# Kernel tuning notes

Hardware: AMD Instinct MI355X
Metric: run time of the kernel (lower is better)

## Reference

```python
import jax, jax.numpy as jnp
import numpy as np

B, L, D = 128, 512, 512   # batch, len_max, encoder feature dim
E, H, V = 64, 512, 17     # label emb size, hidden size, label vocab
PAD = 0                   # entl_pad_value


def setup_inputs() -> dict:
    key = jax.random.key(0)
    ks = jax.random.split(key, 6)
    inputs = jax.random.normal(ks[0], (B, L, D), dtype=jnp.float32)
    emb_table = jax.random.normal(ks[1], (V, E), dtype=jnp.float32) * 0.02
    # xavier_uniform with tanh gain for ht1
    gain = 5.0 / 3.0
    limit1 = gain * np.sqrt(6.0 / (D + E + H))
    W1 = jax.random.uniform(ks[2], (H, D + E), dtype=jnp.float32,
                            minval=-limit1, maxval=limit1)
    b1 = jnp.zeros((H,), dtype=jnp.float32)
    limit2 = np.sqrt(1.0 / H)
    W2 = jax.random.uniform(ks[3], (V, H), dtype=jnp.float32,
                            minval=-limit2, maxval=limit2)
    b2 = jax.random.uniform(ks[4], (V,), dtype=jnp.float32,
                            minval=-limit2, maxval=limit2)
    return {"inputs": inputs, "emb_table": emb_table,
            "W1": W1, "b1": b1, "W2": W2, "b2": b2}


def reference(inputs, emb_table, W1, b1, W2, b2):
    # padding_idx row is identically zero (as in nn.Embedding(padding_idx=PAD))
    table = emb_table.at[PAD].set(0.0)

    def step(prev_emb, x_t):
        # x_t: [B, D], prev_emb: [B, E]
        x = jnp.concatenate([x_t, prev_emb], axis=-1)          # [B, D+E]
        h = jnp.tanh(x @ W1.T + b1)                            # [B, H]
        logit = h @ W2.T + b2                                  # [B, V]
        logp = jax.nn.log_softmax(logit, axis=-1)              # [B, V]
        pred = jnp.argmax(logp, axis=-1)                       # [B] int
        emb = table[pred]                                      # [B, E]
        return emb, (logit, pred, logp, emb)

    init_emb = jnp.broadcast_to(table[PAD], (inputs.shape[0], E))
    xs = jnp.swapaxes(inputs, 0, 1)                            # [L, B, D]
    _, (logits, preds, probs, preds_emb) = jax.lax.scan(step, init_emb, xs)
    # stack along time -> move time to dim 1
    logits = jnp.swapaxes(logits, 0, 1)       # [B, L, V]
    preds = jnp.swapaxes(preds, 0, 1)         # [B, L]
    probs = jnp.swapaxes(probs, 0, 1)         # [B, L, V]
    preds_emb = jnp.swapaxes(preds_emb, 0, 1) # [B, L, E]
    return logits, preds, probs, preds_emb
```

## Files before the change

kernel.cpp:

```cpp
#include <hip/hip_runtime.h>
#include <math.h>

#define B_ 128
#define L_ 512
#define D_ 512
#define E_ 64
#define H_ 512
#define V_ 17

#define LOG2E_F 1.4426950408889634f
#define LN2_F   0.6931471805599453f

__device__ __forceinline__ float fast_tanh(float x) {
  float e = __builtin_amdgcn_exp2f(x * (2.0f * LOG2E_F));
  return 1.0f - 2.0f * __builtin_amdgcn_rcpf(e + 1.0f);
}

__global__ void dh_kernel(const float* __restrict__ W1, const float* __restrict__ table,
                          float* __restrict__ TD) {
  int h = threadIdx.x;
  float w[E_];
#pragma unroll
  for (int e = 0; e < E_; ++e) w[e] = W1[h * (D_ + E_) + D_ + e];
  TD[h] = 0.f;
  for (int v = 1; v < V_; ++v) {
    float acc = 0.f;
#pragma unroll
    for (int e = 0; e < E_; ++e) acc += w[e] * table[v * E_ + e];
    TD[v * H_ + h] = fast_tanh(acc);
  }
}

#define GBM 128
#define GBN 128
#define GBK 32
#define PITCH 20
#define SCALE_A 1024.0f
#define SCALE_W 256.0f
#define INV_SCALE (1.0f / (1024.0f * 256.0f))

typedef _Float16 half8 __attribute__((ext_vector_type(8)));
typedef __fp16 fp16x2 __attribute__((ext_vector_type(2)));
typedef float float4v __attribute__((ext_vector_type(4)));

union H8u { half8 h; fp16x2 p[4]; };

__device__ __forceinline__ uint4 split4(float4 v, float scale) {
  float a0 = v.x * scale, a1 = v.y * scale, a2 = v.z * scale, a3 = v.w * scale;
  _Float16 h0 = (_Float16)a0, h1 = (_Float16)a1, h2 = (_Float16)a2, h3 = (_Float16)a3;
  _Float16 l0 = (_Float16)(a0 - (float)h0), l1 = (_Float16)(a1 - (float)h1);
  _Float16 l2 = (_Float16)(a2 - (float)h2), l3 = (_Float16)(a3 - (float)h3);
  union { _Float16 h; unsigned short u; } c;
  unsigned int hu0, hu1, hu2, hu3, lu0, lu1, lu2, lu3;
  c.h = h0; hu0 = c.u; c.h = h1; hu1 = c.u; c.h = h2; hu2 = c.u; c.h = h3; hu3 = c.u;
  c.h = l0; lu0 = c.u; c.h = l1; lu1 = c.u; c.h = l2; lu2 = c.u; c.h = l3; lu3 = c.u;
  uint4 r;
  r.x = hu0 | (hu1 << 16);
  r.y = hu2 | (hu3 << 16);
  r.z = lu0 | (lu1 << 16);
  r.w = lu2 | (lu3 << 16);
  return r;
}

__global__ __launch_bounds__(256)
void wsplit_kernel(const float* __restrict__ W1, unsigned int* __restrict__ WHI,
                   unsigned int* __restrict__ WLO) {
  const int idx = blockIdx.x * 256 + threadIdx.x;
  const int row = idx >> 7, c4 = idx & 127;
  const float4 wv = *(const float4*)&W1[(size_t)row * (D_ + E_) + 4 * c4];
  const uint4 pw = split4(wv, SCALE_W);
  *(uint2*)&WHI[row * 256 + 2 * c4] = make_uint2(pw.x, pw.y);
  *(uint2*)&WLO[row * 256 + 2 * c4] = make_uint2(pw.z, pw.w);
}

__global__ __launch_bounds__(256, 2)
void gemm_kernel(const float* __restrict__ A, const unsigned int* __restrict__ WHI,
                 const unsigned int* __restrict__ WLO,
                 const float* __restrict__ b1, float* __restrict__ TZ) {
  __shared__ unsigned int Ahi[GBM * PITCH], Alo[GBM * PITCH];
  __shared__ unsigned int Whi[GBN * PITCH], Wlo[GBN * PITCH];

  const int t = threadIdx.x;
  const int ln = t & 63, w = t >> 6;
  const int wm = w & 1, wn = w >> 1;
  const int mBase = blockIdx.x * GBM;
  const int nBase = blockIdx.y * GBN;
  const int lrow = ln & 15, lquad = ln >> 4;

  float4v acc[4][4];
#pragma unroll
  for (int i = 0; i < 4; ++i)
#pragma unroll
    for (int j = 0; j < 4; ++j) acc[i][j] = (float4v){0.f, 0.f, 0.f, 0.f};

  for (int kt = 0; kt < D_; kt += GBK) {
#pragma unroll
    for (int q = 0; q < 4; ++q) {
      const int idx = q * 256 + t;
      const int m = idx >> 3, f = idx & 7;
      const float4 av = *(const float4*)&A[(size_t)(mBase + m) * D_ + kt + 4 * f];
      const uint4 pa = split4(av, SCALE_A);
      *(uint2*)&Ahi[m * PITCH + 2 * f] = make_uint2(pa.x, pa.y);
      *(uint2*)&Alo[m * PITCH + 2 * f] = make_uint2(pa.z, pa.w);
      const uint2 wh = *(const uint2*)&WHI[(nBase + m) * 256 + (kt >> 1) + 2 * f];
      const uint2 wl = *(const uint2*)&WLO[(nBase + m) * 256 + (kt >> 1) + 2 * f];
      *(uint2*)&Whi[m * PITCH + 2 * f] = wh;
      *(uint2*)&Wlo[m * PITCH + 2 * f] = wl;
    }
    __syncthreads();

    half8 ah[4], al[4], bh[4], bl[4];
#pragma unroll
    for (int tm = 0; tm < 4; ++tm) {
      const int off = (wm * 64 + tm * 16 + lrow) * PITCH + 4 * lquad;
      ah[tm] = *(const half8*)&Ahi[off];
      al[tm] = *(const half8*)&Alo[off];
    }
#pragma unroll
    for (int tn = 0; tn < 4; ++tn) {
      const int off = (wn * 64 + tn * 16 + lrow) * PITCH + 4 * lquad;
      bh[tn] = *(const half8*)&Whi[off];
      bl[tn] = *(const half8*)&Wlo[off];
    }
#pragma unroll
    for (int tm = 0; tm < 4; ++tm)
#pragma unroll
      for (int tn = 0; tn < 4; ++tn) {
        acc[tm][tn] = __builtin_amdgcn_mfma_f32_16x16x32_f16(ah[tm], bh[tn], acc[tm][tn], 0, 0, 0);
        acc[tm][tn] = __builtin_amdgcn_mfma_f32_16x16x32_f16(ah[tm], bl[tn], acc[tm][tn], 0, 0, 0);
        acc[tm][tn] = __builtin_amdgcn_mfma_f32_16x16x32_f16(al[tm], bh[tn], acc[tm][tn], 0, 0, 0);
      }
    __syncthreads();
  }

#pragma unroll
  for (int tn = 0; tn < 4; ++tn) {
    const int col = nBase + wn * 64 + tn * 16 + lrow;
    const float bv = b1[col];
#pragma unroll
    for (int tm = 0; tm < 4; ++tm) {
      const int row0 = mBase + wm * 64 + tm * 16 + lquad * 4;
#pragma unroll
      for (int r = 0; r < 4; ++r)
        TZ[(size_t)(row0 + r) * H_ + col] = fast_tanh(acc[tm][tn][r] * INV_SCALE + bv);
    }
  }
}

#define LG_ROWS 32
#define ZP 516
#define WP 260

__global__ __launch_bounds__(512, 2)
void lg_kernel(const float* Zin, const float* __restrict__ TD,
               const float* __restrict__ W2, const float* __restrict__ b2,
               float* G) {
  __shared__ float sTZ[LG_ROWS * ZP];
  __shared__ float sTD[V_ * ZP];
  __shared__ unsigned int sW2hi[16 * WP];
  __shared__ unsigned int sW2lo[16 * WP];
  __shared__ float sW16[H_];
  __shared__ float sS[8][16][20];
  __shared__ unsigned char nb[LG_ROWS][32];

  const int t = threadIdx.x;
  const int ln = t & 63, w = t >> 6;
  const int bt0 = blockIdx.x * LG_ROWS;

#pragma unroll
  for (int i = 0; i < 8; ++i) {
    const int f = t + 512 * i;
    const int r = f >> 7, c = (f & 127) * 4;
    *(float4*)&sTZ[r * ZP + c] = *(const float4*)&Zin[(size_t)(bt0 + r) * H_ + c];
  }
#pragma unroll
  for (int i = 0; i < 5; ++i) {
    const int f = t + 512 * i;
    if (f < (V_ * H_ / 4)) {
      const int r = f >> 7, c = (f & 127) * 4;
      *(float4*)&sTD[r * ZP + c] = *(const float4*)&TD[(size_t)r * H_ + c];
    }
  }
#pragma unroll
  for (int i = 0; i < 4; ++i) {
    const int f = t + 512 * i;
    const int r = f >> 7, c4 = f & 127;
    const float4 wv = *(const float4*)&W2[(size_t)r * H_ + 4 * c4];
    const uint4 pw = split4(wv, SCALE_W);
    *(uint2*)&sW2hi[r * WP + 2 * c4] = make_uint2(pw.x, pw.y);
    *(uint2*)&sW2lo[r * WP + 2 * c4] = make_uint2(pw.z, pw.w);
  }
  if (t < 128) *(float4*)&sW16[t * 4] = *(const float4*)&W2[(size_t)16 * H_ + t * 4];
  __syncthreads();

  const int lrow = ln & 15, lq = ln >> 4;
  const float b2a = b2[lrow];
  const float b2c = b2[16];

  for (int task = w; task < 34; task += 8) {
    const int rg = (task >= 17) ? 1 : 0;
    const int p = task - rg * 17;
    const int rbase = rg * 16;

    float4v acc0 = (float4v){0.f, 0.f, 0.f, 0.f};
    float p16 = 0.f;
    for (int kt = 0; kt < H_; kt += 32) {
      const float* zr = &sTZ[(rbase + lrow) * ZP + kt + lq * 8];
      const float* dr = &sTD[p * ZP + kt + lq * 8];
      float a[8];
#pragma unroll
      for (int j = 0; j < 8; ++j) {
        const float tz = zr[j], td = dr[j];
        const float r = __builtin_amdgcn_rcpf(fmaf(tz, td, 1.0f) * 0.0009765625f);
        a[j] = (tz + td) * r;
      }
      H8u uh, ul;
#pragma unroll
      for (int jj = 0; jj < 4; ++jj) {
        const fp16x2 hp = __builtin_amdgcn_cvt_pkrtz(a[2 * jj], a[2 * jj + 1]);
        uh.p[jj] = hp;
        ul.p[jj] = __builtin_amdgcn_cvt_pkrtz(a[2 * jj] - (float)hp.x,
                                              a[2 * jj + 1] - (float)hp.y);
      }
      const int wo = (kt >> 1) + lq * 4;
      const half8 bh0 = *(const half8*)&sW2hi[lrow * WP + wo];
      const half8 bl0 = *(const half8*)&sW2lo[lrow * WP + wo];
      acc0 = __builtin_amdgcn_mfma_f32_16x16x32_f16(uh.h, bh0, acc0, 0, 0, 0);
      acc0 = __builtin_amdgcn_mfma_f32_16x16x32_f16(uh.h, bl0, acc0, 0, 0, 0);
      acc0 = __builtin_amdgcn_mfma_f32_16x16x32_f16(ul.h, bh0, acc0, 0, 0, 0);
      const float* wr = &sW16[kt + lq * 8];
#pragma unroll
      for (int j = 0; j < 8; ++j) p16 = fmaf(a[j], wr[j], p16);
    }
    p16 += __shfl_xor(p16, 16, 64);
    p16 += __shfl_xor(p16, 32, 64);
#pragma unroll
    for (int r = 0; r < 4; ++r)
      sS[w][lq * 4 + r][lrow] = acc0[r] * INV_SCALE + b2a;
    if (ln < 16) {
      float va[17];
      const float4 q0 = *(const float4*)&sS[w][ln][0];
      const float4 q1 = *(const float4*)&sS[w][ln][4];
      const float4 q2 = *(const float4*)&sS[w][ln][8];
      const float4 q3 = *(const float4*)&sS[w][ln][12];
      va[0] = q0.x; va[1] = q0.y; va[2] = q0.z; va[3] = q0.w;
      va[4] = q1.x; va[5] = q1.y; va[6] = q1.z; va[7] = q1.w;
      va[8] = q2.x; va[9] = q2.y; va[10] = q2.z; va[11] = q2.w;
      va[12] = q3.x; va[13] = q3.y; va[14] = q3.z; va[15] = q3.w;
      va[16] = p16 * (1.0f / 1024.0f) + b2c;
      float m = va[0]; int am = 0;
#pragma unroll
      for (int i = 1; i < 17; ++i) if (va[i] > m) { m = va[i]; am = i; }
      float* gs = &G[(size_t)(bt0 + rbase + ln) * H_ + p * 20];
      *(float4*)&gs[0] = q0; *(float4*)&gs[4] = q1;
      *(float4*)&gs[8] = q2; *(float4*)&gs[12] = q3;
      gs[16] = va[16];
      nb[rbase + ln][p] = (unsigned char)am;
    }
  }
  __syncthreads();
  if (t < 160) {
    const int row = t / 5, d = t % 5;
    ((unsigned int*)&G[(size_t)(bt0 + row) * H_ + 352])[d] =
        *(const unsigned int*)&nb[row][d * 4];
  }
}

__global__ __launch_bounds__(64, 1)
void chase_kernel(const float* __restrict__ G, float* __restrict__ out_preds) {
  __shared__ unsigned char nxt[L_ * 32];
  const int b = blockIdx.x, ln = threadIdx.x;
#pragma unroll
  for (int i = 0; i < 8; ++i) {
    const int tt = ln + 64 * i;
    const unsigned int* src = (const unsigned int*)&G[((size_t)b * L_ + tt) * H_ + 352];
    *(uint4*)&nxt[tt * 32] = *(const uint4*)src;
    *(unsigned int*)&nxt[tt * 32 + 16] = src[4];
  }
  __syncthreads();
  int pred = 0;
  float* op = out_preds + (size_t)b * L_;
  for (int tt = 0; tt < L_; ++tt) {
    pred = nxt[tt * 32 + pred];
    if (ln == 0) op[tt] = (float)pred;
  }
}

__global__ __launch_bounds__(256)
void epi_kernel(const float* __restrict__ G, const float* __restrict__ table,
                const float* __restrict__ preds,
                float* __restrict__ out_logits, float* __restrict__ out_probs,
                float* __restrict__ out_pemb) {
  const int bt = blockIdx.x * 256 + threadIdx.x;
  const int tt = bt & (L_ - 1);
  const int p = (tt == 0) ? 0 : (int)preds[bt - 1];
  const float* g = &G[(size_t)bt * H_ + p * 20];
  float va[17];
  {
    const float4 q0 = *(const float4*)&g[0];
    const float4 q1 = *(const float4*)&g[4];
    const float4 q2 = *(const float4*)&g[8];
    const float4 q3 = *(const float4*)&g[12];
    va[0] = q0.x; va[1] = q0.y; va[2] = q0.z; va[3] = q0.w;
    va[4] = q1.x; va[5] = q1.y; va[6] = q1.z; va[7] = q1.w;
    va[8] = q2.x; va[9] = q2.y; va[10] = q2.z; va[11] = q2.w;
    va[12] = q3.x; va[13] = q3.y; va[14] = q3.z; va[15] = q3.w;
    va[16] = g[16];
  }
  float m = va[0];
#pragma unroll
  for (int i = 1; i < 17; ++i) m = fmaxf(m, va[i]);
  float s = 0.f;
#pragma unroll
  for (int i = 0; i < 17; ++i) s += __builtin_amdgcn_exp2f((va[i] - m) * LOG2E_F);
  const float lse = __builtin_amdgcn_logf(s) * LN2_F;
  float* lo = out_logits + (size_t)bt * V_;
  float* pb = out_probs + (size_t)bt * V_;
#pragma unroll
  for (int i = 0; i < 17; ++i) { lo[i] = va[i]; pb[i] = va[i] - m - lse; }
  const int pr = (int)preds[bt];
  float* pe = out_pemb + (size_t)bt * E_;
  if (pr == 0) {
#pragma unroll
    for (int i = 0; i < 16; ++i) *(float4*)&pe[4 * i] = (float4){0.f, 0.f, 0.f, 0.f};
  } else {
    const float* tr = &table[(size_t)pr * E_];
#pragma unroll
    for (int i = 0; i < 16; ++i) *(float4*)&pe[4 * i] = *(const float4*)&tr[4 * i];
  }
}

extern "C" void kernel_launch(void* const* d_in, const int* in_sizes, int n_in,
                              void* d_out, int out_size, void* d_ws, size_t ws_size,
                              hipStream_t stream) {
  const float* inputs = (const float*)d_in[0];
  const float* table  = (const float*)d_in[1];
  const float* W1     = (const float*)d_in[2];
  const float* b1     = (const float*)d_in[3];
  const float* W2     = (const float*)d_in[4];
  const float* b2     = (const float*)d_in[5];

  float* out = (float*)d_out;
  float* out_logits = out;
  float* out_preds  = out_logits + (size_t)B_ * L_ * V_;
  float* out_probs  = out_preds + (size_t)B_ * L_;
  float* out_pemb   = out_probs + (size_t)B_ * L_ * V_;

  float* TD = (float*)d_ws;
  float* TZ = (float*)((char*)d_ws + 65536);

  unsigned int* WHI = (unsigned int*)out_pemb;
  unsigned int* WLO = WHI + 512 * 256;

  dh_kernel<<<1, 512, 0, stream>>>(W1, table, TD);
  wsplit_kernel<<<256, 256, 0, stream>>>(W1, WHI, WLO);
  dim3 g(65536 / GBM, H_ / GBN);
  gemm_kernel<<<g, 256, 0, stream>>>(inputs, WHI, WLO, b1, TZ);
  lg_kernel<<<65536 / LG_ROWS, 512, 0, stream>>>(TZ, TD, W2, b2, TZ);
  chase_kernel<<<B_, 64, 0, stream>>>(TZ, out_preds);
  epi_kernel<<<65536 / 256, 256, 0, stream>>>(TZ, table, out_preds,
                                              out_logits, out_probs, out_pemb);
}
```

Baseline: 572.8 us.

## Widen GEMM tile to full N and rework logit kernel with fp16 tanh-addition expansion

The hidden GEMM now uses 512-thread blocks that each compute all 512 output columns for 128 rows, so every A tile is loaded and split once per block instead of once per N-block. The logit kernel stores the tanh activations pre-split into fp16 hi/lo parts plus a derivative term. It replaces the per-element fp32 reciprocal of the tanh-addition formula with an fp16 series correction added to the low part, and precomputes the base row-16 dot product once per row. Each wave now processes up to five label candidates with a shared A fragment. This cuts VALU work and reloads, at the cost of more registers and LDS and of reduced accuracy from the fp16 polynomial approximation.

```diff
diff --git a/kernel.cpp b/kernel.cpp
--- a/kernel.cpp
+++ b/kernel.cpp
@@ -31,9 +31,6 @@
   }
 }
 
-#define GBM 128
-#define GBN 128
-#define GBK 32
 #define PITCH 20
 #define SCALE_A 1024.0f
 #define SCALE_W 256.0f
@@ -43,7 +40,7 @@
 typedef __fp16 fp16x2 __attribute__((ext_vector_type(2)));
 typedef float float4v __attribute__((ext_vector_type(4)));
 
-union H8u { half8 h; fp16x2 p[4]; };
+union H8c { half8 h; fp16x2 q[4]; unsigned int u[4]; uint4 u4; };
 
 __device__ __forceinline__ uint4 split4(float4 v, float scale) {
   float a0 = v.x * scale, a1 = v.y * scale, a2 = v.z * scale, a3 = v.w * scale;
@@ -62,6 +59,14 @@
   return r;
 }
 
+__device__ __forceinline__ uint2 pack4h(_Float16 a, _Float16 b, _Float16 c, _Float16 d) {
+  union { _Float16 h; unsigned short u; } x;
+  unsigned int lo, hi;
+  x.h = a; lo = x.u; x.h = b; lo |= ((unsigned int)x.u) << 16;
+  x.h = c; hi = x.u; x.h = d; hi |= ((unsigned int)x.u) << 16;
+  return make_uint2(lo, hi);
+}
+
 __global__ __launch_bounds__(256)
 void wsplit_kernel(const float* __restrict__ W1, unsigned int* __restrict__ WHI,
                    unsigned int* __restrict__ WLO) {
@@ -73,43 +78,45 @@
   *(uint2*)&WLO[row * 256 + 2 * c4] = make_uint2(pw.z, pw.w);
 }
 
-__global__ __launch_bounds__(256, 2)
+__global__ __launch_bounds__(512, 2)
 void gemm_kernel(const float* __restrict__ A, const unsigned int* __restrict__ WHI,
                  const unsigned int* __restrict__ WLO,
                  const float* __restrict__ b1, float* __restrict__ TZ) {
-  __shared__ unsigned int Ahi[GBM * PITCH], Alo[GBM * PITCH];
-  __shared__ unsigned int Whi[GBN * PITCH], Wlo[GBN * PITCH];
+  __shared__ unsigned int Ahi[128 * PITCH], Alo[128 * PITCH];
+  __shared__ unsigned int Whi[512 * PITCH], Wlo[512 * PITCH];
 
   const int t = threadIdx.x;
   const int ln = t & 63, w = t >> 6;
   const int wm = w & 1, wn = w >> 1;
-  const int mBase = blockIdx.x * GBM;
-  const int nBase = blockIdx.y * GBN;
+  const int mBase = blockIdx.x * 128;
   const int lrow = ln & 15, lquad = ln >> 4;
 
-  float4v acc[4][4];
+  float4v acc[4][8];
 #pragma unroll
   for (int i = 0; i < 4; ++i)
 #pragma unroll
-    for (int j = 0; j < 4; ++j) acc[i][j] = (float4v){0.f, 0.f, 0.f, 0.f};
-
-  for (int kt = 0; kt < D_; kt += GBK) {
-#pragma unroll
-    for (int q = 0; q < 4; ++q) {
-      const int idx = q * 256 + t;
+    for (int j = 0; j < 8; ++j) acc[i][j] = (float4v){0.f, 0.f, 0.f, 0.f};
+
+  for (int kt = 0; kt < D_; kt += 32) {
+#pragma unroll
+    for (int q = 0; q < 2; ++q) {
+      const int idx = q * 512 + t;
       const int m = idx >> 3, f = idx & 7;
       const float4 av = *(const float4*)&A[(size_t)(mBase + m) * D_ + kt + 4 * f];
       const uint4 pa = split4(av, SCALE_A);
       *(uint2*)&Ahi[m * PITCH + 2 * f] = make_uint2(pa.x, pa.y);
       *(uint2*)&Alo[m * PITCH + 2 * f] = make_uint2(pa.z, pa.w);
-      const uint2 wh = *(const uint2*)&WHI[(nBase + m) * 256 + (kt >> 1) + 2 * f];
-      const uint2 wl = *(const uint2*)&WLO[(nBase + m) * 256 + (kt >> 1) + 2 * f];
-      *(uint2*)&Whi[m * PITCH + 2 * f] = wh;
-      *(uint2*)&Wlo[m * PITCH + 2 * f] = wl;
+    }
+#pragma unroll
+    for (int q = 0; q < 4; ++q) {
+      const int idx = q * 512 + t;
+      const int n = idx >> 2, d4 = (idx & 3) * 4;
+      *(uint4*)&Whi[n * PITCH + d4] = *(const uint4*)&WHI[n * 256 + (kt >> 1) + d4];
+      *(uint4*)&Wlo[n * PITCH + d4] = *(const uint4*)&WLO[n * 256 + (kt >> 1) + d4];
     }
     __syncthreads();
 
-    half8 ah[4], al[4], bh[4], bl[4];
+    half8 ah[4], al[4];
 #pragma unroll
     for (int tm = 0; tm < 4; ++tm) {
       const int off = (wm * 64 + tm * 16 + lrow) * PITCH + 4 * lquad;
@@ -117,25 +124,23 @@
       al[tm] = *(const half8*)&Alo[off];
     }
 #pragma unroll
-    for (int tn = 0; tn < 4; ++tn) {
-      const int off = (wn * 64 + tn * 16 + lrow) * PITCH + 4 * lquad;
-      bh[tn] = *(const half8*)&Whi[off];
-      bl[tn] = *(const half8*)&Wlo[off];
-    }
-#pragma unroll
-    for (int tm = 0; tm < 4; ++tm)
-#pragma unroll
-      for (int tn = 0; tn < 4; ++tn) {
-        acc[tm][tn] = __builtin_amdgcn_mfma_f32_16x16x32_f16(ah[tm], bh[tn], acc[tm][tn], 0, 0, 0);
-        acc[tm][tn] = __builtin_amdgcn_mfma_f32_16x16x32_f16(ah[tm], bl[tn], acc[tm][tn], 0, 0, 0);
-        acc[tm][tn] = __builtin_amdgcn_mfma_f32_16x16x32_f16(al[tm], bh[tn], acc[tm][tn], 0, 0, 0);
+    for (int tn = 0; tn < 8; ++tn) {
+      const int off = (wn * 128 + tn * 16 + lrow) * PITCH + 4 * lquad;
+      const half8 bh = *(const half8*)&Whi[off];
+      const half8 bl = *(const half8*)&Wlo[off];
+#pragma unroll
+      for (int tm = 0; tm < 4; ++tm) {
+        acc[tm][tn] = __builtin_amdgcn_mfma_f32_16x16x32_f16(ah[tm], bh, acc[tm][tn], 0, 0, 0);
+        acc[tm][tn] = __builtin_amdgcn_mfma_f32_16x16x32_f16(ah[tm], bl, acc[tm][tn], 0, 0, 0);
+        acc[tm][tn] = __builtin_amdgcn_mfma_f32_16x16x32_f16(al[tm], bh, acc[tm][tn], 0, 0, 0);
       }
+    }
     __syncthreads();
   }
 
 #pragma unroll
-  for (int tn = 0; tn < 4; ++tn) {
-    const int col = nBase + wn * 64 + tn * 16 + lrow;
+  for (int tn = 0; tn < 8; ++tn) {
+    const int col = wn * 128 + tn * 16 + lrow;
     const float bv = b1[col];
 #pragma unroll
     for (int tm = 0; tm < 4; ++tm) {
@@ -147,38 +152,54 @@
   }
 }
 
-#define LG_ROWS 32
-#define ZP 516
+#define LGR 32
+#define AP 520
 #define WP 260
 
 __global__ __launch_bounds__(512, 2)
 void lg_kernel(const float* Zin, const float* __restrict__ TD,
                const float* __restrict__ W2, const float* __restrict__ b2,
                float* G) {
-  __shared__ float sTZ[LG_ROWS * ZP];
-  __shared__ float sTD[V_ * ZP];
-  __shared__ unsigned int sW2hi[16 * WP];
-  __shared__ unsigned int sW2lo[16 * WP];
-  __shared__ float sW16[H_];
-  __shared__ float sS[8][16][20];
-  __shared__ unsigned char nb[LG_ROWS][32];
+  __shared__ __align__(16) unsigned int sAhiD[LGR * AP / 2];
+  __shared__ __align__(16) unsigned int sAloD[LGR * AP / 2];
+  __shared__ __align__(16) unsigned int sUD[LGR * AP / 2];
+  __shared__ __align__(16) unsigned int sTDd[V_ * 256];
+  __shared__ __align__(16) unsigned int sW2hi[16 * WP];
+  __shared__ __align__(16) unsigned int sW2lo[16 * WP];
+  __shared__ __align__(16) unsigned int sW16hi[256];
+  __shared__ __align__(16) unsigned int sW16lo[256];
+  __shared__ __align__(16) float sS[8][16][20];
+  __shared__ __align__(16) float sV16b[32];
+  __shared__ __align__(16) unsigned char nb[LGR][20];
 
   const int t = threadIdx.x;
   const int ln = t & 63, w = t >> 6;
-  const int bt0 = blockIdx.x * LG_ROWS;
+  const int bt0 = blockIdx.x * LGR;
 
 #pragma unroll
   for (int i = 0; i < 8; ++i) {
     const int f = t + 512 * i;
-    const int r = f >> 7, c = (f & 127) * 4;
-    *(float4*)&sTZ[r * ZP + c] = *(const float4*)&Zin[(size_t)(bt0 + r) * H_ + c];
+    const int r = f >> 7, c4 = f & 127;
+    const float4 z = *(const float4*)&Zin[(size_t)(bt0 + r) * H_ + 4 * c4];
+    const float a0 = 1024.f * z.x, a1 = 1024.f * z.y, a2 = 1024.f * z.z, a3 = 1024.f * z.w;
+    const _Float16 h0 = (_Float16)a0, h1 = (_Float16)a1, h2 = (_Float16)a2, h3 = (_Float16)a3;
+    const _Float16 l0 = (_Float16)(a0 - (float)h0), l1 = (_Float16)(a1 - (float)h1);
+    const _Float16 l2 = (_Float16)(a2 - (float)h2), l3 = (_Float16)(a3 - (float)h3);
+    const _Float16 u0 = (_Float16)fmaf(-a0, z.x, 1024.f), u1 = (_Float16)fmaf(-a1, z.y, 1024.f);
+    const _Float16 u2 = (_Float16)fmaf(-a2, z.z, 1024.f), u3 = (_Float16)fmaf(-a3, z.w, 1024.f);
+    const int o = r * (AP / 2) + 2 * c4;
+    *(uint2*)&sAhiD[o] = pack4h(h0, h1, h2, h3);
+    *(uint2*)&sAloD[o] = pack4h(l0, l1, l2, l3);
+    *(uint2*)&sUD[o]   = pack4h(u0, u1, u2, u3);
   }
 #pragma unroll
   for (int i = 0; i < 5; ++i) {
     const int f = t + 512 * i;
-    if (f < (V_ * H_ / 4)) {
-      const int r = f >> 7, c = (f & 127) * 4;
-      *(float4*)&sTD[r * ZP + c] = *(const float4*)&TD[(size_t)r * H_ + c];
+    if (f < V_ * 128) {
+      const int r = f >> 7, c4 = f & 127;
+      const float4 d = *(const float4*)&TD[(size_t)r * H_ + 4 * c4];
+      *(uint2*)&sTDd[r * 256 + 2 * c4] =
+          pack4h((_Float16)d.x, (_Float16)d.y, (_Float16)d.z, (_Float16)d.w);
     }
   }
 #pragma unroll
@@ -190,72 +211,119 @@
     *(uint2*)&sW2hi[r * WP + 2 * c4] = make_uint2(pw.x, pw.y);
     *(uint2*)&sW2lo[r * WP + 2 * c4] = make_uint2(pw.z, pw.w);
   }
-  if (t < 128) *(float4*)&sW16[t * 4] = *(const float4*)&W2[(size_t)16 * H_ + t * 4];
+  if (t < 128) {
+    const float4 wv = *(const float4*)&W2[(size_t)16 * H_ + 4 * t];
+    const uint4 pw = split4(wv, 1.0f);
+    *(uint2*)&sW16hi[2 * t] = make_uint2(pw.x, pw.y);
+    *(uint2*)&sW16lo[2 * t] = make_uint2(pw.z, pw.w);
+  }
   __syncthreads();
 
+  {
+    const int row = t >> 4, seg = t & 15;
+    const unsigned int* Ah = &sAhiD[row * (AP / 2) + seg * 16];
+    const unsigned int* Al = &sAloD[row * (AP / 2) + seg * 16];
+    const unsigned int* Wh = &sW16hi[seg * 16];
+    const unsigned int* Wl = &sW16lo[seg * 16];
+    float s = 0.f;
+#pragma unroll
+    for (int j = 0; j < 16; ++j) {
+      const fp16x2 a = __builtin_bit_cast(fp16x2, Ah[j]);
+      const fp16x2 l = __builtin_bit_cast(fp16x2, Al[j]);
+      const fp16x2 wh = __builtin_bit_cast(fp16x2, Wh[j]);
+      const fp16x2 wl = __builtin_bit_cast(fp16x2, Wl[j]);
+      s = __builtin_amdgcn_fdot2(a, wh, s, false);
+      s = __builtin_amdgcn_fdot2(l, wh, s, false);
+      s = __builtin_amdgcn_fdot2(a, wl, s, false);
+    }
+    ((float*)sS)[row * 16 + seg] = s;
+  }
+  __syncthreads();
+  if (t < 32) {
+    float s = 0.f;
+#pragma unroll
+    for (int j = 0; j < 16; ++j) s += ((float*)sS)[t * 16 + j];
+    sV16b[t] = s;
+  }
+  __syncthreads();
+
   const int lrow = ln & 15, lq = ln >> 4;
+  const int rg = w & 1, pq = w >> 1;
+  const int rbase = rg * 16;
   const float b2a = b2[lrow];
   const float b2c = b2[16];
 
-  for (int task = w; task < 34; task += 8) {
-    const int rg = (task >= 17) ? 1 : 0;
-    const int p = task - rg * 17;
-    const int rbase = rg * 16;
-
-    float4v acc0 = (float4v){0.f, 0.f, 0.f, 0.f};
-    float p16 = 0.f;
-    for (int kt = 0; kt < H_; kt += 32) {
-      const float* zr = &sTZ[(rbase + lrow) * ZP + kt + lq * 8];
-      const float* dr = &sTD[p * ZP + kt + lq * 8];
-      float a[8];
-#pragma unroll
-      for (int j = 0; j < 8; ++j) {
-        const float tz = zr[j], td = dr[j];
-        const float r = __builtin_amdgcn_rcpf(fmaf(tz, td, 1.0f) * 0.0009765625f);
-        a[j] = (tz + td) * r;
+  float4v acc[5];
+  float p16s[5];
+#pragma unroll
+  for (int pi = 0; pi < 5; ++pi) { acc[pi] = (float4v){0.f, 0.f, 0.f, 0.f}; p16s[pi] = 0.f; }
+
+  const _Float16* Ahalf = (const _Float16*)sAhiD;
+  const _Float16* Alhalf = (const _Float16*)sAloD;
+  const _Float16* Uhalf = (const _Float16*)sUD;
+  const _Float16* TDhalf = (const _Float16*)sTDd;
+
+  for (int kt = 0; kt < H_; kt += 32) {
+    const int ho = kt + lq * 8;
+    const half8 ahi = *(const half8*)(Ahalf + (rbase + lrow) * AP + ho);
+    const half8 alo = *(const half8*)(Alhalf + (rbase + lrow) * AP + ho);
+    const half8 uu  = *(const half8*)(Uhalf + (rbase + lrow) * AP + ho);
+    const half8 tzv = ahi * (_Float16)0.0009765625f;
+    H8c W16f; W16f.u4 = *(const uint4*)&sW16hi[ho >> 1];
+    const int wo = lrow * WP + (kt >> 1) + lq * 4;
+    const half8 bh0 = *(const half8*)&sW2hi[wo];
+    const half8 bl0 = *(const half8*)&sW2lo[wo];
+#pragma unroll
+    for (int pi = 0; pi < 5; ++pi) {
+      const int p = pq + 4 * pi;
+      if (p < V_) {
+        const half8 td = *(const half8*)(TDhalf + p * 512 + ho);
+        const half8 q = tzv * td;
+        const half8 s = q * q + ((_Float16)1.0f - q);
+        const half8 dl = uu * (td * s);
+        const half8 alp = alo + dl;
+        acc[pi] = __builtin_amdgcn_mfma_f32_16x16x32_f16(ahi, bh0, acc[pi], 0, 0, 0);
+        acc[pi] = __builtin_amdgcn_mfma_f32_16x16x32_f16(ahi, bl0, acc[pi], 0, 0, 0);
+        acc[pi] = __builtin_amdgcn_mfma_f32_16x16x32_f16(alp, bh0, acc[pi], 0, 0, 0);
+        H8c DL; DL.h = dl;
+        p16s[pi] = __builtin_amdgcn_fdot2(DL.q[0], W16f.q[0], p16s[pi], false);
+        p16s[pi] = __builtin_amdgcn_fdot2(DL.q[1], W16f.q[1], p16s[pi], false);
+        p16s[pi] = __builtin_amdgcn_fdot2(DL.q[2], W16f.q[2], p16s[pi], false);
+        p16s[pi] = __builtin_amdgcn_fdot2(DL.q[3], W16f.q[3], p16s[pi], false);
       }
-      H8u uh, ul;
-#pragma unroll
-      for (int jj = 0; jj < 4; ++jj) {
-        const fp16x2 hp = __builtin_amdgcn_cvt_pkrtz(a[2 * jj], a[2 * jj + 1]);
-        uh.p[jj] = hp;
-        ul.p[jj] = __builtin_amdgcn_cvt_pkrtz(a[2 * jj] - (float)hp.x,
-                                              a[2 * jj + 1] - (float)hp.y);
+    }
+  }
+
+#pragma unroll
+  for (int pi = 0; pi < 5; ++pi) {
+    const int p = pq + 4 * pi;
+    if (p < V_) {
+      float p16 = p16s[pi];
+      p16 += __shfl_xor(p16, 16, 64);
+      p16 += __shfl_xor(p16, 32, 64);
+#pragma unroll
+      for (int r = 0; r < 4; ++r)
+        sS[w][lq * 4 + r][lrow] = acc[pi][r] * INV_SCALE + b2a;
+      if (ln < 16) {
+        float va[17];
+        const float4 q0 = *(const float4*)&sS[w][ln][0];
+        const float4 q1 = *(const float4*)&sS[w][ln][4];
+        const float4 q2 = *(const float4*)&sS[w][ln][8];
+        const float4 q3 = *(const float4*)&sS[w][ln][12];
+        va[0] = q0.x; va[1] = q0.y; va[2] = q0.z; va[3] = q0.w;
+        va[4] = q1.x; va[5] = q1.y; va[6] = q1.z; va[7] = q1.w;
+        va[8] = q2.x; va[9] = q2.y; va[10] = q2.z; va[11] = q2.w;
+        va[12] = q3.x; va[13] = q3.y; va[14] = q3.z; va[15] = q3.w;
+        va[16] = (sV16b[rbase + ln] + p16) * 0.0009765625f + b2c;
+        float m = va[0]; int am = 0;
+#pragma unroll
+        for (int i = 1; i < 17; ++i) if (va[i] > m) { m = va[i]; am = i; }
+        float* gs = &G[(size_t)(bt0 + rbase + ln) * H_ + p * 20];
+        *(float4*)&gs[0] = q0; *(float4*)&gs[4] = q1;
+        *(float4*)&gs[8] = q2; *(float4*)&gs[12] = q3;
+        gs[16] = va[16];
+        nb[rbase + ln][p] = (unsigned char)am;
       }
-      const int wo = (kt >> 1) + lq * 4;
-      const half8 bh0 = *(const half8*)&sW2hi[lrow * WP + wo];
-      const half8 bl0 = *(const half8*)&sW2lo[lrow * WP + wo];
-      acc0 = __builtin_amdgcn_mfma_f32_16x16x32_f16(uh.h, bh0, acc0, 0, 0, 0);
-      acc0 = __builtin_amdgcn_mfma_f32_16x16x32_f16(uh.h, bl0, acc0, 0, 0, 0);
-      acc0 = __builtin_amdgcn_mfma_f32_16x16x32_f16(ul.h, bh0, acc0, 0, 0, 0);
-      const float* wr = &sW16[kt + lq * 8];
-#pragma unroll
-      for (int j = 0; j < 8; ++j) p16 = fmaf(a[j], wr[j], p16);
-    }
-    p16 += __shfl_xor(p16, 16, 64);
-    p16 += __shfl_xor(p16, 32, 64);
-#pragma unroll
-    for (int r = 0; r < 4; ++r)
-      sS[w][lq * 4 + r][lrow] = acc0[r] * INV_SCALE + b2a;
-    if (ln < 16) {
-      float va[17];
-      const float4 q0 = *(const float4*)&sS[w][ln][0];
-      const float4 q1 = *(const float4*)&sS[w][ln][4];
-      const float4 q2 = *(const float4*)&sS[w][ln][8];
-      const float4 q3 = *(const float4*)&sS[w][ln][12];
-      va[0] = q0.x; va[1] = q0.y; va[2] = q0.z; va[3] = q0.w;
-      va[4] = q1.x; va[5] = q1.y; va[6] = q1.z; va[7] = q1.w;
-      va[8] = q2.x; va[9] = q2.y; va[10] = q2.z; va[11] = q2.w;
-      va[12] = q3.x; va[13] = q3.y; va[14] = q3.z; va[15] = q3.w;
-      va[16] = p16 * (1.0f / 1024.0f) + b2c;
-      float m = va[0]; int am = 0;
-#pragma unroll
-      for (int i = 1; i < 17; ++i) if (va[i] > m) { m = va[i]; am = i; }
-      float* gs = &G[(size_t)(bt0 + rbase + ln) * H_ + p * 20];
-      *(float4*)&gs[0] = q0; *(float4*)&gs[4] = q1;
-      *(float4*)&gs[8] = q2; *(float4*)&gs[12] = q3;
-      gs[16] = va[16];
-      nb[rbase + ln][p] = (unsigned char)am;
     }
   }
   __syncthreads();
@@ -354,9 +422,8 @@
 
   dh_kernel<<<1, 512, 0, stream>>>(W1, table, TD);
   wsplit_kernel<<<256, 256, 0, stream>>>(W1, WHI, WLO);
-  dim3 g(65536 / GBM, H_ / GBN);
-  gemm_kernel<<<g, 256, 0, stream>>>(inputs, WHI, WLO, b1, TZ);
-  lg_kernel<<<65536 / LG_ROWS, 512, 0, stream>>>(TZ, TD, W2, b2, TZ);
+  gemm_kernel<<<512, 512, 0, stream>>>(inputs, WHI, WLO, b1, TZ);
+  lg_kernel<<<65536 / LGR, 512, 0, stream>>>(TZ, TD, W2, b2, TZ);
   chase_kernel<<<B_, 64, 0, stream>>>(TZ, out_preds);
   epi_kernel<<<65536 / 256, 256, 0, stream>>>(TZ, table, out_preds,
                                               out_logits, out_probs, out_pemb);
```

New measurement: 502.4 us. 12.3% less time.
